# Performance work log

Measured on AMD Instinct MI355X. Metric: run time of the kernel, lower is better.

The kernel has to match this reference:

```python
import jax, jax.numpy as jnp
import numpy as np

B, T, C = 2, 2048, 1024
N_HEAD = 16
HEAD_DIM = C // N_HEAD
ROPE_BASE = 10000.0


def setup_inputs() -> dict:
    key = jax.random.key(0)
    ks = jax.random.split(key, 5)
    s = 0.02
    return {
        "x": jax.random.normal(ks[0], (B, T, C), dtype=jnp.float32),
        "Wq": jax.random.normal(ks[1], (C, C), dtype=jnp.float32) * s,
        "Wk": jax.random.normal(ks[2], (C, C), dtype=jnp.float32) * s,
        "Wv": jax.random.normal(ks[3], (C, C), dtype=jnp.float32) * s,
        "Wo": jax.random.normal(ks[4], (C, C), dtype=jnp.float32) * s,
    }


def _rope_cos_sin(seq_len, head_dim, dtype):
    inv_freq = 1.0 / (ROPE_BASE ** (jnp.arange(0, head_dim, 2, dtype=jnp.float32) / head_dim))
    t = jnp.arange(seq_len, dtype=jnp.float32)
    freqs = jnp.einsum("i,j->ij", t, inv_freq)          # [T, head_dim/2]
    emb = jnp.concatenate([freqs, freqs], axis=-1)        # [T, head_dim]
    return jnp.cos(emb).astype(dtype), jnp.sin(emb).astype(dtype)


def _rotate_half(x):
    x1, x2 = jnp.split(x, 2, axis=-1)
    return jnp.concatenate([-x2, x1], axis=-1)


def _mha(x, Wq, Wk, Wv, Wo):
    b, t, c = x.shape
    # torch nn.Linear stores weight [out, in]: y = x @ W.T
    q = (x @ Wq.T).reshape(b, t, N_HEAD, HEAD_DIM).transpose(0, 2, 1, 3)  # [B,H,T,D]
    k = (x @ Wk.T).reshape(b, t, N_HEAD, HEAD_DIM).transpose(0, 2, 1, 3)
    v = (x @ Wv.T).reshape(b, t, N_HEAD, HEAD_DIM).transpose(0, 2, 1, 3)
    cos, sin = _rope_cos_sin(t, HEAD_DIM, x.dtype)        # [T,D] each, broadcast over B,H
    q = q * cos + _rotate_half(q) * sin
    k = k * cos + _rotate_half(k) * sin
    scale = 1.0 / np.sqrt(HEAD_DIM).astype(np.float32)
    att = jnp.einsum("bhqd,bhkd->bhqk", q, k) * scale     # [B,H,T,T]
    causal = jnp.tril(jnp.ones((t, t), dtype=bool))
    att = jnp.where(causal, att, jnp.finfo(att.dtype).min)
    att = jax.nn.softmax(att, axis=-1)
    y = jnp.einsum("bhqk,bhkd->bhqd", att, v)             # [B,H,T,D]
    y = y.transpose(0, 2, 1, 3).reshape(b, t, c)
    return y @ Wo.T


def reference(x, Wq, Wk, Wv, Wo):
    return _mha(x, Wq, Wk, Wv, Wo)
```

## Files before the change

### kernel.cpp

```cpp
#include <hip/hip_runtime.h>

#define BB 2
#define TT 2048
#define CC 1024
#define NH 16
#define HD 64

typedef __attribute__((ext_vector_type(8))) short bf16x8;
typedef __attribute__((ext_vector_type(4))) float floatx4;
typedef __attribute__((ext_vector_type(16))) float floatx16;

__device__ __forceinline__ unsigned short f2bf(float f) {
    union { float f; unsigned int u; } v; v.f = f;
    unsigned int u = v.u;
    u = (u + 0x7fffu + ((u >> 16) & 1u)) >> 16;
    return (unsigned short)u;
}
__device__ __forceinline__ float bf2f(unsigned short u) {
    return __uint_as_float((unsigned)u << 16);
}

typedef __attribute__((address_space(3))) unsigned char* lds_ptr_t;
typedef const __attribute__((address_space(1))) unsigned char* glob_ptr_t;
__device__ __forceinline__ void gll16(const void* g, void* l) {
    __builtin_amdgcn_global_load_lds((glob_ptr_t)g, (lds_ptr_t)l, 16, 0, 0);
}

__global__ __launch_bounds__(256) void cast_all_k(const float* __restrict__ x,
                                                  const float* __restrict__ wq,
                                                  const float* __restrict__ wk,
                                                  const float* __restrict__ wv,
                                                  const float* __restrict__ wo,
                                                  unsigned short* __restrict__ xb,
                                                  unsigned short* __restrict__ wqkvb,
                                                  unsigned short* __restrict__ wob,
                                                  float2* __restrict__ tabQ,
                                                  float2* __restrict__ tabK) {
    if (blockIdx.x >= 8192) {
        int idx = (blockIdx.x - 8192) * 256 + threadIdx.x;
        int t = idx >> 5, j = idx & 31;
        const float C1 = 0.41524101186092f;
        const float I2PI = 0.15915494309189535f;
        float rev = (float)t * (__builtin_amdgcn_exp2f(-(float)j * C1) * I2PI);
        rev -= floorf(rev);
        float ang = rev * 6.2831853071796f;
        float c = __cosf(ang), s = __sinf(ang);
        const float qs = 0.18033688011112f;
        tabK[idx] = make_float2(c, s);
        tabQ[idx] = make_float2(c * qs, s * qs);
        return;
    }
    int i = blockIdx.x * 256 + threadIdx.x;
    const float* src;
    unsigned short* dst;
    if (i < 1048576) {
        src = x + (size_t)i * 4;
        dst = xb + (size_t)i * 4;
    } else {
        int w   = (i - 1048576) >> 18;
        int off = (i - 1048576) & 262143;
        const float* s0 = (w == 0) ? wq : (w == 1) ? wk : (w == 2) ? wv : wo;
        unsigned short* d0 = (w == 3) ? wob : (wqkvb + (size_t)w * 1048576);
        src = s0 + (size_t)off * 4;
        dst = d0 + (size_t)off * 4;
    }
    float4 v = *(const float4*)src;
    ushort4 o;
    o.x = f2bf(v.x); o.y = f2bf(v.y); o.z = f2bf(v.z); o.w = f2bf(v.w);
    *(ushort4*)dst = o;
}

__global__ __launch_bounds__(256) void gemm128_k(const unsigned short* __restrict__ A,
                                                 const unsigned short* __restrict__ Bt,
                                                 float* __restrict__ C, int N, int K) {
    __shared__ __align__(16) unsigned short As[128][32];
    __shared__ __align__(16) unsigned short Bs[128][32];
    const int tid  = threadIdx.x;
    const int wave = tid >> 6;
    const int lane = tid & 63;
    const int quad = lane >> 4;
    const int l16  = lane & 15;
    const int wr = (wave >> 1) * 64;
    const int wc = (wave & 1) * 64;
    const int bid = blockIdx.x;
    const int xcd = bid & 7, sl = bid >> 3;
    const int row0 = (xcd * 4 + (sl >> 3)) * 128;
    const int col0 = (sl & 7) * 128;
    const int srow = tid >> 2;
    const int scol = (tid & 3) * 8;

    const unsigned short* Ap0 = A  + (size_t)(row0 + srow) * K + scol;
    const unsigned short* Ap1 = A  + (size_t)(row0 + 64 + srow) * K + scol;
    const unsigned short* Bp0 = Bt + (size_t)(col0 + srow) * K + scol;
    const unsigned short* Bp1 = Bt + (size_t)(col0 + 64 + srow) * K + scol;

    floatx4 acc[4][4];
    #pragma unroll
    for (int i = 0; i < 4; i++)
        #pragma unroll
        for (int j = 0; j < 4; j++) acc[i][j] = (floatx4){0.f, 0.f, 0.f, 0.f};

    for (int k0 = 0; k0 < K; k0 += 32) {
        __syncthreads();
        gll16(Ap0 + k0, &As[srow][scol]);
        gll16(Ap1 + k0, &As[64 + srow][scol]);
        gll16(Bp0 + k0, &Bs[srow][scol]);
        gll16(Bp1 + k0, &Bs[64 + srow][scol]);
        __syncthreads();
        bf16x8 af[4], bfr[4];
        #pragma unroll
        for (int i = 0; i < 4; i++) af[i]  = *(const bf16x8*)&As[wr + 16 * i + l16][quad * 8];
        #pragma unroll
        for (int j = 0; j < 4; j++) bfr[j] = *(const bf16x8*)&Bs[wc + 16 * j + l16][quad * 8];
        #pragma unroll
        for (int i = 0; i < 4; i++)
            #pragma unroll
            for (int j = 0; j < 4; j++)
                acc[i][j] = __builtin_amdgcn_mfma_f32_16x16x32_bf16(af[i], bfr[j], acc[i][j], 0, 0, 0);
    }

    #pragma unroll
    for (int i = 0; i < 4; i++)
        #pragma unroll
        for (int j = 0; j < 4; j++)
            #pragma unroll
            for (int r = 0; r < 4; r++) {
                int row = row0 + wr + 16 * i + quad * 4 + r;
                int col = col0 + wc + 16 * j + l16;
                C[(size_t)row * N + col] = acc[i][j][r];
            }
}

__global__ __launch_bounds__(256) void gemm_qkv_k(const unsigned short* __restrict__ A,
                                                  const unsigned short* __restrict__ Bt,
                                                  const float2* __restrict__ tabQ,
                                                  const float2* __restrict__ tabK,
                                                  unsigned short* __restrict__ Qb,
                                                  unsigned short* __restrict__ Kb,
                                                  unsigned short* __restrict__ Vb) {
    __shared__ __align__(16) unsigned short SMEM[128 * 128];
    unsigned short (*As)[32] = (unsigned short(*)[32])SMEM;
    unsigned short (*Bs)[32] = (unsigned short(*)[32])(SMEM + 128 * 32);
    unsigned short (*Eb)[128] = (unsigned short(*)[128])SMEM;
    const int K = 1024;
    const int tid  = threadIdx.x;
    const int wave = tid >> 6;
    const int lane = tid & 63;
    const int quad = lane >> 4;
    const int l16  = lane & 15;
    const int wr = (wave >> 1) * 64;
    const int wc = (wave & 1) * 64;
    const int bid = blockIdx.x;
    const int xcd = bid & 7, sl = bid >> 3;
    const int row0 = (xcd * 4 + sl / 24) * 128;
    const int col0 = (sl % 24) * 128;
    const int srow = tid >> 2;
    const int scol = (tid & 3) * 8;

    const unsigned short* Ap0 = A  + (size_t)(row0 + srow) * K + scol;
    const unsigned short* Ap1 = A  + (size_t)(row0 + 64 + srow) * K + scol;
    const unsigned short* Bp0 = Bt + (size_t)(col0 + srow) * K + scol;
    const unsigned short* Bp1 = Bt + (size_t)(col0 + 64 + srow) * K + scol;

    floatx4 acc[4][4];
    #pragma unroll
    for (int i = 0; i < 4; i++)
        #pragma unroll
        for (int j = 0; j < 4; j++) acc[i][j] = (floatx4){0.f, 0.f, 0.f, 0.f};

    for (int k0 = 0; k0 < K; k0 += 32) {
        __syncthreads();
        gll16(Ap0 + k0, &As[srow][scol]);
        gll16(Ap1 + k0, &As[64 + srow][scol]);
        gll16(Bp0 + k0, &Bs[srow][scol]);
        gll16(Bp1 + k0, &Bs[64 + srow][scol]);
        __syncthreads();
        bf16x8 af[4], bfr[4];
        #pragma unroll
        for (int i = 0; i < 4; i++) af[i]  = *(const bf16x8*)&As[wr + 16 * i + l16][quad * 8];
        #pragma unroll
        for (int j = 0; j < 4; j++) bfr[j] = *(const bf16x8*)&Bs[wc + 16 * j + l16][quad * 8];
        #pragma unroll
        for (int i = 0; i < 4; i++)
            #pragma unroll
            for (int j = 0; j < 4; j++)
                acc[i][j] = __builtin_amdgcn_mfma_f32_16x16x32_bf16(af[i], bfr[j], acc[i][j], 0, 0, 0);
    }

    __syncthreads();
    #pragma unroll
    for (int i = 0; i < 4; i++)
        #pragma unroll
        for (int j = 0; j < 4; j++)
            #pragma unroll
            for (int r = 0; r < 4; r++) {
                int erow = wr + 16 * i + quad * 4 + r;
                int col  = wc + 16 * j + l16;
                int pcol = (((col >> 3) ^ (erow & 15)) << 3) | (col & 7);
                Eb[erow][pcol] = f2bf(acc[i][j][r]);
            }
    __syncthreads();

    const int row  = tid >> 1;
    const int half = tid & 1;
    const int grow = row0 + row;
    const int t    = grow & (TT - 1);
    const int bb   = grow >> 11;
    const int sect = col0 >> 10;
    const int hh   = ((col0 & 1023) >> 6) + half;
    union { int4 q[8]; unsigned short u[64]; } raw;
    #pragma unroll
    for (int i = 0; i < 8; i++) {
        int pg = (half * 8 + i) ^ (row & 15);
        raw.q[i] = *(const int4*)&Eb[row][pg << 3];
    }
    size_t obase = ((size_t)(bb * NH + hh) * TT + t) * 64;
    if (sect == 2) {
        #pragma unroll
        for (int i = 0; i < 8; i++) *(int4*)(Vb + obase + 8 * i) = raw.q[i];
    } else {
        const float4* tab = (const float4*)((sect ? tabK : tabQ) + (size_t)t * 32);
        unsigned short* dst = sect ? Kb : Qb;
        union { int4 q[8]; unsigned short u[64]; } o;
        #pragma unroll
        for (int i = 0; i < 16; i++) {
            float4 cs = tab[i];
            int j0 = 2 * i, j1 = 2 * i + 1;
            float a0 = bf2f(raw.u[j0]), b0 = bf2f(raw.u[j0 + 32]);
            float a1 = bf2f(raw.u[j1]), b1 = bf2f(raw.u[j1 + 32]);
            o.u[j0]      = f2bf(a0 * cs.x - b0 * cs.y);
            o.u[j0 + 32] = f2bf(b0 * cs.x + a0 * cs.y);
            o.u[j1]      = f2bf(a1 * cs.z - b1 * cs.w);
            o.u[j1 + 32] = f2bf(b1 * cs.z + a1 * cs.w);
        }
        #pragma unroll
        for (int i = 0; i < 8; i++) *(int4*)(dst + obase + 8 * i) = o.q[i];
    }
}

__global__ __launch_bounds__(256) void vtr_k(const unsigned short* __restrict__ Vb,
                                             unsigned short* __restrict__ Vt) {
    __shared__ __align__(16) unsigned short Vsh[64][70];
    const int tid = threadIdx.x;
    const int tt = blockIdx.x;
    const int bh = blockIdx.y;
    const int sr = tid >> 2;
    const int sc = (tid & 3) * 16;
    const unsigned short* src = Vb + ((size_t)bh * TT + tt * 64 + sr) * 64 + sc;
    *(int4*)&Vsh[sr][sc]     = *(const int4*)src;
    *(int4*)&Vsh[sr][sc + 8] = *(const int4*)(src + 8);
    __syncthreads();
    const int dr = tid >> 2;
    const int tc = (tid & 3) * 16;
    unsigned short tv[16];
    #pragma unroll
    for (int i = 0; i < 16; i++) {
        int x = tc + i;
        int key = (x & ~15) + (x & 3) + ((x >> 2) & 1) * 8 + ((x >> 3) & 1) * 4;
        tv[i] = Vsh[key][dr];
    }
    size_t vo = ((size_t)bh * 64 + dr) * TT + tt * 64 + tc;
    *(int4*)(Vt + vo)     = *(int4*)&tv[0];
    *(int4*)(Vt + vo + 8) = *(int4*)&tv[8];
}

__global__ __launch_bounds__(256, 4) void flash_k(const unsigned short* __restrict__ Qb,
                                                  const unsigned short* __restrict__ Kb,
                                                  const unsigned short* __restrict__ Vt,
                                                  unsigned short* __restrict__ O0,
                                                  unsigned short* __restrict__ O1,
                                                  float* __restrict__ L0, float* __restrict__ L1) {
    __shared__ __align__(16) unsigned short Ks[64][72];
    __shared__ __align__(16) unsigned short Vs[64][72];
    const int tid  = threadIdx.x;
    const int wave = tid >> 6;
    const int lane = tid & 63;
    const int h    = lane >> 5;
    const int l32  = lane & 31;
    const int qt    = 15 - (blockIdx.x >> 6);
    const int inner = blockIdx.x & 63;
    const int bh    = inner >> 1;
    const int split = inner & 1;
    const int q0 = qt * 128;
    const int qw = q0 + wave * 32 + l32;
    const int sr = tid >> 2;
    const int sc = (tid & 3) * 16;

    bf16x8 qf[4];
    {
        const unsigned short* qp = Qb + ((size_t)bh * TT + qw) * 64 + h * 8;
        #pragma unroll
        for (int kk = 0; kk < 4; kk++) qf[kk] = *(const bf16x8*)(qp + kk * 16);
    }

    floatx16 accO[2];
    accO[0] = (floatx16)(0.f);
    accO[1] = (floatx16)(0.f);
    float lsum = 0.f;

    const int kt0 = split * (qt + 1);
    const int kt1 = kt0 + qt + 1;
    const unsigned short* kbase = Kb + (size_t)bh * TT * 64;
    const unsigned short* vbase = Vt + (size_t)bh * 64 * TT;

    const unsigned short* kp = kbase + ((size_t)(kt0 * 64) + sr) * 64 + sc;
    const unsigned short* vp = vbase + (size_t)sr * TT + kt0 * 64 + sc;
    int4 ka = *(const int4*)kp, kb2 = *(const int4*)(kp + 8);
    int4 va = *(const int4*)vp, vb2 = *(const int4*)(vp + 8);

    for (int kt = kt0; kt < kt1; kt++) {
        __syncthreads();
        *(int4*)&Ks[sr][sc]     = ka;
        *(int4*)&Ks[sr][sc + 8] = kb2;
        *(int4*)&Vs[sr][sc]     = va;
        *(int4*)&Vs[sr][sc + 8] = vb2;
        __syncthreads();
        if (kt + 1 < kt1) {
            const unsigned short* kp2 = kbase + ((size_t)((kt + 1) * 64) + sr) * 64 + sc;
            const unsigned short* vp2 = vbase + (size_t)sr * TT + (kt + 1) * 64 + sc;
            ka  = *(const int4*)kp2; kb2 = *(const int4*)(kp2 + 8);
            va  = *(const int4*)vp2; vb2 = *(const int4*)(vp2 + 8);
        }

        const bool diag = (kt >= 2 * qt);
        bf16x8 pfrag[4];

        #pragma unroll
        for (int mb = 0; mb < 2; mb++) {
            floatx16 sacc = (floatx16)(0.f);
            #pragma unroll
            for (int kk = 0; kk < 4; kk++) {
                bf16x8 kf = *(const bf16x8*)&Ks[32 * mb + l32][kk * 16 + h * 8];
                sacc = __builtin_amdgcn_mfma_f32_32x32x16_bf16(kf, qf[kk], sacc, 0, 0, 0);
            }
            float p[16];
            const int kmb = kt * 64 + 32 * mb + 4 * h;
            #pragma unroll
            for (int r = 0; r < 16; r++) {
                float pv = __builtin_amdgcn_exp2f(sacc[r]);
                if (diag) {
                    int ki = kmb + (r & 3) + 8 * (r >> 2);
                    if (ki > qw) pv = 0.f;
                }
                lsum += pv;
                p[r] = pv;
            }
            #pragma unroll
            for (int half = 0; half < 2; half++) {
                union { bf16x8 v; unsigned u[4]; } pk;
                #pragma unroll
                for (int i = 0; i < 4; i++) {
                    unsigned ulo = __float_as_uint(p[half * 8 + 2 * i]);
                    unsigned uhi = __float_as_uint(p[half * 8 + 2 * i + 1]);
                    pk.u[i] = (ulo >> 16) | (uhi & 0xffff0000u);
                }
                pfrag[2 * mb + half] = pk.v;
            }
        }

        #pragma unroll
        for (int mbo = 0; mbo < 2; mbo++) {
            #pragma unroll
            for (int kk = 0; kk < 4; kk++) {
                bf16x8 vf = *(const bf16x8*)&Vs[32 * mbo + l32][kk * 16 + h * 8];
                accO[mbo] = __builtin_amdgcn_mfma_f32_32x32x16_bf16(vf, pfrag[kk], accO[mbo], 0, 0, 0);
            }
        }
    }

    lsum += __shfl_xor(lsum, 32);
    unsigned short* Op = split ? O1 : O0;
    float* Lp = split ? L1 : L0;
    if (lane < 32) Lp[(size_t)bh * TT + qw] = lsum;
    unsigned short* orow = Op + ((size_t)bh * TT + qw) * 64;
    #pragma unroll
    for (int mbo = 0; mbo < 2; mbo++)
        #pragma unroll
        for (int a = 0; a < 4; a++) {
            ushort4 o4;
            o4.x = f2bf(accO[mbo][4 * a + 0]);
            o4.y = f2bf(accO[mbo][4 * a + 1]);
            o4.z = f2bf(accO[mbo][4 * a + 2]);
            o4.w = f2bf(accO[mbo][4 * a + 3]);
            *(ushort4*)(orow + 32 * mbo + 8 * a + 4 * h) = o4;
        }
}

__global__ __launch_bounds__(256) void combine_k(const unsigned short* __restrict__ O0,
                                                 const unsigned short* __restrict__ O1,
                                                 const float* __restrict__ L0,
                                                 const float* __restrict__ L1,
                                                 unsigned short* __restrict__ Yb) {
    int idx = blockIdx.x * 256 + threadIdx.x;
    int dg  = idx & 15;
    int row = idx >> 4;
    float inv = 1.0f / (L0[row] + L1[row]);
    uint2 a = ((const uint2*)O0)[idx];
    uint2 b = ((const uint2*)O1)[idx];
    float a0 = __uint_as_float(a.x << 16),      b0 = __uint_as_float(b.x << 16);
    float a1 = __uint_as_float(a.x & 0xffff0000u), b1 = __uint_as_float(b.x & 0xffff0000u);
    float a2 = __uint_as_float(a.y << 16),      b2 = __uint_as_float(b.y << 16);
    float a3 = __uint_as_float(a.y & 0xffff0000u), b3 = __uint_as_float(b.y & 0xffff0000u);
    ushort4 o;
    o.x = f2bf((a0 + b0) * inv);
    o.y = f2bf((a1 + b1) * inv);
    o.z = f2bf((a2 + b2) * inv);
    o.w = f2bf((a3 + b3) * inv);
    int bh = row >> 11, t = row & (TT - 1);
    int bb = bh >> 4, hh = bh & 15;
    *(ushort4*)(Yb + ((size_t)(bb * TT + t)) * CC + hh * 64 + dg * 4) = o;
}

extern "C" void kernel_launch(void* const* d_in, const int* in_sizes, int n_in,
                              void* d_out, int out_size, void* d_ws, size_t ws_size,
                              hipStream_t stream) {
    (void)in_sizes; (void)n_in; (void)out_size; (void)ws_size;
    const float* x  = (const float*)d_in[0];
    const float* Wq = (const float*)d_in[1];
    const float* Wk = (const float*)d_in[2];
    const float* Wv = (const float*)d_in[3];
    const float* Wo = (const float*)d_in[4];
    float* out = (float*)d_out;
    char* ws = (char*)d_ws;

    unsigned short* xb    = (unsigned short*)(ws + 0);
    unsigned short* wqkvb = (unsigned short*)(ws + (8ull  << 20));
    unsigned short* wob   = (unsigned short*)(ws + (14ull << 20));
    unsigned short* Qb    = (unsigned short*)(ws + (16ull << 20));
    unsigned short* Kb    = (unsigned short*)(ws + (24ull << 20));
    unsigned short* Vb    = (unsigned short*)(ws + (32ull << 20));
    unsigned short* Vt    = (unsigned short*)(ws + (40ull << 20));
    unsigned short* Yb    = (unsigned short*)(ws + (48ull << 20));
    unsigned short* O0    = (unsigned short*)(ws + (56ull << 20));
    unsigned short* O1    = (unsigned short*)(ws + (64ull << 20));
    float* L0 = (float*)(ws + (72ull << 20));
    float* L1 = (float*)(ws + (72ull << 20) + (256ull << 10));
    float2* tabQ = (float2*)(ws + (73ull << 20));
    float2* tabK = (float2*)(ws + (73ull << 20) + (512ull << 10));

    cast_all_k<<<8448, 256, 0, stream>>>(x, Wq, Wk, Wv, Wo, xb, wqkvb, wob, tabQ, tabK);
    gemm_qkv_k<<<768, 256, 0, stream>>>(xb, wqkvb, tabQ, tabK, Qb, Kb, Vb);
    vtr_k<<<dim3(32, 32), 256, 0, stream>>>(Vb, Vt);
    flash_k<<<1024, 256, 0, stream>>>(Qb, Kb, Vt, O0, O1, L0, L1);
    combine_k<<<4096, 256, 0, stream>>>(O0, O1, L0, L1, Yb);
    gemm128_k<<<256, 256, 0, stream>>>(Yb, wob, out, 1024, 1024);
}
```

Baseline: 192.0 us.

## Deepen GEMM K-tile with XOR-swizzled LDS and use 128-key flash tiles

Both GEMM kernels now stage 64-wide K slices instead of 32, with an XOR swizzle on the LDS column groups so the fragment reads avoid bank conflicts. This halves the number of barrier pairs per K sweep. The flash attention kernel now stages 128-key K/V tiles per iteration and splits each query tile's key range roughly in half between the two splits, cutting loop iterations and barriers. In exchange it uses more LDS and registers, so flash occupancy drops to 3 blocks per SIMD, and the diagonal masking now covers a full 128-key tile.

New measurement: 219.5 us. +14.3%, slower.

```diff
diff --git a/kernel.cpp b/kernel.cpp
--- a/kernel.cpp
+++ b/kernel.cpp
@@ -73,26 +73,26 @@
 __global__ __launch_bounds__(256) void gemm128_k(const unsigned short* __restrict__ A,
                                                  const unsigned short* __restrict__ Bt,
                                                  float* __restrict__ C, int N, int K) {
-    __shared__ __align__(16) unsigned short As[128][32];
-    __shared__ __align__(16) unsigned short Bs[128][32];
+    __shared__ __align__(16) unsigned short As[128][64];
+    __shared__ __align__(16) unsigned short Bs[128][64];
     const int tid  = threadIdx.x;
     const int wave = tid >> 6;
     const int lane = tid & 63;
     const int quad = lane >> 4;
     const int l16  = lane & 15;
+    const int sw   = l16 & 7;
     const int wr = (wave >> 1) * 64;
     const int wc = (wave & 1) * 64;
     const int bid = blockIdx.x;
     const int xcd = bid & 7, sl = bid >> 3;
     const int row0 = (xcd * 4 + (sl >> 3)) * 128;
     const int col0 = (sl & 7) * 128;
-    const int srow = tid >> 2;
-    const int scol = (tid & 3) * 8;
-
-    const unsigned short* Ap0 = A  + (size_t)(row0 + srow) * K + scol;
-    const unsigned short* Ap1 = A  + (size_t)(row0 + 64 + srow) * K + scol;
-    const unsigned short* Bp0 = Bt + (size_t)(col0 + srow) * K + scol;
-    const unsigned short* Bp1 = Bt + (size_t)(col0 + 64 + srow) * K + scol;
+    const int w8r = wave * 8 + (lane >> 3);
+    const int cg  = ((lane & 7) ^ (lane >> 3)) * 8;
+    const int cl  = (lane & 7) * 8;
+
+    const unsigned short* Ap = A  + (size_t)(row0 + w8r) * K + cg;
+    const unsigned short* Bp = Bt + (size_t)(col0 + w8r) * K + cg;
 
     floatx4 acc[4][4];
     #pragma unroll
@@ -100,23 +100,29 @@
         #pragma unroll
         for (int j = 0; j < 4; j++) acc[i][j] = (floatx4){0.f, 0.f, 0.f, 0.f};
 
-    for (int k0 = 0; k0 < K; k0 += 32) {
-        __syncthreads();
-        gll16(Ap0 + k0, &As[srow][scol]);
-        gll16(Ap1 + k0, &As[64 + srow][scol]);
-        gll16(Bp0 + k0, &Bs[srow][scol]);
-        gll16(Bp1 + k0, &Bs[64 + srow][scol]);
-        __syncthreads();
-        bf16x8 af[4], bfr[4];
-        #pragma unroll
-        for (int i = 0; i < 4; i++) af[i]  = *(const bf16x8*)&As[wr + 16 * i + l16][quad * 8];
-        #pragma unroll
-        for (int j = 0; j < 4; j++) bfr[j] = *(const bf16x8*)&Bs[wc + 16 * j + l16][quad * 8];
-        #pragma unroll
-        for (int i = 0; i < 4; i++)
+    for (int k0 = 0; k0 < K; k0 += 64) {
+        __syncthreads();
+        #pragma unroll
+        for (int isu = 0; isu < 4; isu++) {
+            gll16(Ap + (size_t)(isu * 32) * K + k0, &As[isu * 32 + w8r][cl]);
+            gll16(Bp + (size_t)(isu * 32) * K + k0, &Bs[isu * 32 + w8r][cl]);
+        }
+        __syncthreads();
+        #pragma unroll
+        for (int kk = 0; kk < 2; kk++) {
+            bf16x8 af[4], bfr[4];
+            #pragma unroll
+            for (int i = 0; i < 4; i++)
+                af[i]  = *(const bf16x8*)&As[wr + 16 * i + l16][((kk * 4 + quad) ^ sw) * 8];
             #pragma unroll
             for (int j = 0; j < 4; j++)
-                acc[i][j] = __builtin_amdgcn_mfma_f32_16x16x32_bf16(af[i], bfr[j], acc[i][j], 0, 0, 0);
+                bfr[j] = *(const bf16x8*)&Bs[wc + 16 * j + l16][((kk * 4 + quad) ^ sw) * 8];
+            #pragma unroll
+            for (int i = 0; i < 4; i++)
+                #pragma unroll
+                for (int j = 0; j < 4; j++)
+                    acc[i][j] = __builtin_amdgcn_mfma_f32_16x16x32_bf16(af[i], bfr[j], acc[i][j], 0, 0, 0);
+        }
     }
 
     #pragma unroll
@@ -139,8 +145,8 @@
                                                   unsigned short* __restrict__ Kb,
                                                   unsigned short* __restrict__ Vb) {
     __shared__ __align__(16) unsigned short SMEM[128 * 128];
-    unsigned short (*As)[32] = (unsigned short(*)[32])SMEM;
-    unsigned short (*Bs)[32] = (unsigned short(*)[32])(SMEM + 128 * 32);
+    unsigned short (*As)[64] = (unsigned short(*)[64])SMEM;
+    unsigned short (*Bs)[64] = (unsigned short(*)[64])(SMEM + 128 * 64);
     unsigned short (*Eb)[128] = (unsigned short(*)[128])SMEM;
     const int K = 1024;
     const int tid  = threadIdx.x;
@@ -148,19 +154,19 @@
     const int lane = tid & 63;
     const int quad = lane >> 4;
     const int l16  = lane & 15;
+    const int sw   = l16 & 7;
     const int wr = (wave >> 1) * 64;
     const int wc = (wave & 1) * 64;
     const int bid = blockIdx.x;
     const int xcd = bid & 7, sl = bid >> 3;
     const int row0 = (xcd * 4 + sl / 24) * 128;
     const int col0 = (sl % 24) * 128;
-    const int srow = tid >> 2;
-    const int scol = (tid & 3) * 8;
-
-    const unsigned short* Ap0 = A  + (size_t)(row0 + srow) * K + scol;
-    const unsigned short* Ap1 = A  + (size_t)(row0 + 64 + srow) * K + scol;
-    const unsigned short* Bp0 = Bt + (size_t)(col0 + srow) * K + scol;
-    const unsigned short* Bp1 = Bt + (size_t)(col0 + 64 + srow) * K + scol;
+    const int w8r = wave * 8 + (lane >> 3);
+    const int cg  = ((lane & 7) ^ (lane >> 3)) * 8;
+    const int cl  = (lane & 7) * 8;
+
+    const unsigned short* Ap = A  + (size_t)(row0 + w8r) * K + cg;
+    const unsigned short* Bp = Bt + (size_t)(col0 + w8r) * K + cg;
 
     floatx4 acc[4][4];
     #pragma unroll
@@ -168,23 +174,29 @@
         #pragma unroll
         for (int j = 0; j < 4; j++) acc[i][j] = (floatx4){0.f, 0.f, 0.f, 0.f};
 
-    for (int k0 = 0; k0 < K; k0 += 32) {
-        __syncthreads();
-        gll16(Ap0 + k0, &As[srow][scol]);
-        gll16(Ap1 + k0, &As[64 + srow][scol]);
-        gll16(Bp0 + k0, &Bs[srow][scol]);
-        gll16(Bp1 + k0, &Bs[64 + srow][scol]);
-        __syncthreads();
-        bf16x8 af[4], bfr[4];
-        #pragma unroll
-        for (int i = 0; i < 4; i++) af[i]  = *(const bf16x8*)&As[wr + 16 * i + l16][quad * 8];
-        #pragma unroll
-        for (int j = 0; j < 4; j++) bfr[j] = *(const bf16x8*)&Bs[wc + 16 * j + l16][quad * 8];
-        #pragma unroll
-        for (int i = 0; i < 4; i++)
+    for (int k0 = 0; k0 < K; k0 += 64) {
+        __syncthreads();
+        #pragma unroll
+        for (int isu = 0; isu < 4; isu++) {
+            gll16(Ap + (size_t)(isu * 32) * K + k0, &As[isu * 32 + w8r][cl]);
+            gll16(Bp + (size_t)(isu * 32) * K + k0, &Bs[isu * 32 + w8r][cl]);
+        }
+        __syncthreads();
+        #pragma unroll
+        for (int kk = 0; kk < 2; kk++) {
+            bf16x8 af[4], bfr[4];
+            #pragma unroll
+            for (int i = 0; i < 4; i++)
+                af[i]  = *(const bf16x8*)&As[wr + 16 * i + l16][((kk * 4 + quad) ^ sw) * 8];
             #pragma unroll
             for (int j = 0; j < 4; j++)
-                acc[i][j] = __builtin_amdgcn_mfma_f32_16x16x32_bf16(af[i], bfr[j], acc[i][j], 0, 0, 0);
+                bfr[j] = *(const bf16x8*)&Bs[wc + 16 * j + l16][((kk * 4 + quad) ^ sw) * 8];
+            #pragma unroll
+            for (int i = 0; i < 4; i++)
+                #pragma unroll
+                for (int j = 0; j < 4; j++)
+                    acc[i][j] = __builtin_amdgcn_mfma_f32_16x16x32_bf16(af[i], bfr[j], acc[i][j], 0, 0, 0);
+        }
     }
 
     __syncthreads();
@@ -264,14 +276,14 @@
     *(int4*)(Vt + vo + 8) = *(int4*)&tv[8];
 }
 
-__global__ __launch_bounds__(256, 4) void flash_k(const unsigned short* __restrict__ Qb,
+__global__ __launch_bounds__(256, 3) void flash_k(const unsigned short* __restrict__ Qb,
                                                   const unsigned short* __restrict__ Kb,
                                                   const unsigned short* __restrict__ Vt,
                                                   unsigned short* __restrict__ O0,
                                                   unsigned short* __restrict__ O1,
                                                   float* __restrict__ L0, float* __restrict__ L1) {
-    __shared__ __align__(16) unsigned short Ks[64][72];
-    __shared__ __align__(16) unsigned short Vs[64][72];
+    __shared__ __align__(16) unsigned short Ks[128][72];
+    __shared__ __align__(16) unsigned short Vs[64][136];
     const int tid  = threadIdx.x;
     const int wave = tid >> 6;
     const int lane = tid & 63;
@@ -283,8 +295,10 @@
     const int split = inner & 1;
     const int q0 = qt * 128;
     const int qw = q0 + wave * 32 + l32;
-    const int sr = tid >> 2;
-    const int sc = (tid & 3) * 16;
+    const int kr = tid >> 1;
+    const int kc = (tid & 1) * 32;
+    const int vr = tid >> 2;
+    const int vc = (tid & 3) * 32;
 
     bf16x8 qf[4];
     {
@@ -298,72 +312,82 @@
     accO[1] = (floatx16)(0.f);
     float lsum = 0.f;
 
-    const int kt0 = split * (qt + 1);
-    const int kt1 = kt0 + qt + 1;
+    const int n128 = qt + 1;
+    const int s0 = (n128 + 1) >> 1;
+    const int m0 = split ? s0 : 0;
+    const int m1 = split ? n128 : s0;
     const unsigned short* kbase = Kb + (size_t)bh * TT * 64;
     const unsigned short* vbase = Vt + (size_t)bh * 64 * TT;
 
-    const unsigned short* kp = kbase + ((size_t)(kt0 * 64) + sr) * 64 + sc;
-    const unsigned short* vp = vbase + (size_t)sr * TT + kt0 * 64 + sc;
-    int4 ka = *(const int4*)kp, kb2 = *(const int4*)(kp + 8);
-    int4 va = *(const int4*)vp, vb2 = *(const int4*)(vp + 8);
-
-    for (int kt = kt0; kt < kt1; kt++) {
-        __syncthreads();
-        *(int4*)&Ks[sr][sc]     = ka;
-        *(int4*)&Ks[sr][sc + 8] = kb2;
-        *(int4*)&Vs[sr][sc]     = va;
-        *(int4*)&Vs[sr][sc + 8] = vb2;
-        __syncthreads();
-        if (kt + 1 < kt1) {
-            const unsigned short* kp2 = kbase + ((size_t)((kt + 1) * 64) + sr) * 64 + sc;
-            const unsigned short* vp2 = vbase + (size_t)sr * TT + (kt + 1) * 64 + sc;
-            ka  = *(const int4*)kp2; kb2 = *(const int4*)(kp2 + 8);
-            va  = *(const int4*)vp2; vb2 = *(const int4*)(vp2 + 8);
-        }
-
-        const bool diag = (kt >= 2 * qt);
-        bf16x8 pfrag[4];
-
-        #pragma unroll
-        for (int mb = 0; mb < 2; mb++) {
-            floatx16 sacc = (floatx16)(0.f);
-            #pragma unroll
-            for (int kk = 0; kk < 4; kk++) {
-                bf16x8 kf = *(const bf16x8*)&Ks[32 * mb + l32][kk * 16 + h * 8];
-                sacc = __builtin_amdgcn_mfma_f32_32x32x16_bf16(kf, qf[kk], sacc, 0, 0, 0);
+    int4 kreg[4], vreg[4];
+    if (m0 < m1) {
+        const unsigned short* kp = kbase + ((size_t)(m0 * 128) + kr) * 64 + kc;
+        const unsigned short* vp = vbase + (size_t)vr * TT + m0 * 128 + vc;
+        #pragma unroll
+        for (int i = 0; i < 4; i++) kreg[i] = *(const int4*)(kp + 8 * i);
+        #pragma unroll
+        for (int i = 0; i < 4; i++) vreg[i] = *(const int4*)(vp + 8 * i);
+    }
+
+    for (int m = m0; m < m1; m++) {
+        __syncthreads();
+        #pragma unroll
+        for (int i = 0; i < 4; i++) *(int4*)&Ks[kr][kc + 8 * i] = kreg[i];
+        #pragma unroll
+        for (int i = 0; i < 4; i++) *(int4*)&Vs[vr][vc + 8 * i] = vreg[i];
+        __syncthreads();
+        if (m + 1 < m1) {
+            const unsigned short* kp = kbase + ((size_t)((m + 1) * 128) + kr) * 64 + kc;
+            const unsigned short* vp = vbase + (size_t)vr * TT + (m + 1) * 128 + vc;
+            #pragma unroll
+            for (int i = 0; i < 4; i++) kreg[i] = *(const int4*)(kp + 8 * i);
+            #pragma unroll
+            for (int i = 0; i < 4; i++) vreg[i] = *(const int4*)(vp + 8 * i);
+        }
+
+        const bool diag = (m == qt);
+        #pragma unroll
+        for (int sub = 0; sub < 2; sub++) {
+            bf16x8 pfrag[4];
+            #pragma unroll
+            for (int mb = 0; mb < 2; mb++) {
+                floatx16 sacc = (floatx16)(0.f);
+                #pragma unroll
+                for (int kk = 0; kk < 4; kk++) {
+                    bf16x8 kf = *(const bf16x8*)&Ks[sub * 64 + 32 * mb + l32][kk * 16 + h * 8];
+                    sacc = __builtin_amdgcn_mfma_f32_32x32x16_bf16(kf, qf[kk], sacc, 0, 0, 0);
+                }
+                float p[16];
+                const int kmb = m * 128 + sub * 64 + 32 * mb + 4 * h;
+                #pragma unroll
+                for (int r = 0; r < 16; r++) {
+                    float pv = __builtin_amdgcn_exp2f(sacc[r]);
+                    if (diag) {
+                        int ki = kmb + (r & 3) + 8 * (r >> 2);
+                        if (ki > qw) pv = 0.f;
+                    }
+                    lsum += pv;
+                    p[r] = pv;
+                }
+                #pragma unroll
+                for (int hf = 0; hf < 2; hf++) {
+                    union { bf16x8 v; unsigned u[4]; } pk;
+                    #pragma unroll
+                    for (int i = 0; i < 4; i++) {
+                        unsigned ulo = __float_as_uint(p[hf * 8 + 2 * i]);
+                        unsigned uhi = __float_as_uint(p[hf * 8 + 2 * i + 1]);
+                        pk.u[i] = (ulo >> 16) | (uhi & 0xffff0000u);
+                    }
+                    pfrag[2 * mb + hf] = pk.v;
+                }
             }
-            float p[16];
-            const int kmb = kt * 64 + 32 * mb + 4 * h;
-            #pragma unroll
-            for (int r = 0; r < 16; r++) {
-                float pv = __builtin_amdgcn_exp2f(sacc[r]);
-                if (diag) {
-                    int ki = kmb + (r & 3) + 8 * (r >> 2);
-                    if (ki > qw) pv = 0.f;
+            #pragma unroll
+            for (int mbo = 0; mbo < 2; mbo++) {
+                #pragma unroll
+                for (int kk = 0; kk < 4; kk++) {
+                    bf16x8 vf = *(const bf16x8*)&Vs[32 * mbo + l32][sub * 64 + kk * 16 + h * 8];
+                    accO[mbo] = __builtin_amdgcn_mfma_f32_32x32x16_bf16(vf, pfrag[kk], accO[mbo], 0, 0, 0);
                 }
-                lsum += pv;
-                p[r] = pv;
-            }
-            #pragma unroll
-            for (int half = 0; half < 2; half++) {
-                union { bf16x8 v; unsigned u[4]; } pk;
-                #pragma unroll
-                for (int i = 0; i < 4; i++) {
-                    unsigned ulo = __float_as_uint(p[half * 8 + 2 * i]);
-                    unsigned uhi = __float_as_uint(p[half * 8 + 2 * i + 1]);
-                    pk.u[i] = (ulo >> 16) | (uhi & 0xffff0000u);
-                }
-                pfrag[2 * mb + half] = pk.v;
-            }
-        }
-
-        #pragma unroll
-        for (int mbo = 0; mbo < 2; mbo++) {
-            #pragma unroll
-            for (int kk = 0; kk < 4; kk++) {
-                bf16x8 vf = *(const bf16x8*)&Vs[32 * mbo + l32][kk * 16 + h * 8];
-                accO[mbo] = __builtin_amdgcn_mfma_f32_32x32x16_bf16(vf, pfrag[kk], accO[mbo], 0, 0, 0);
             }
         }
     }
```
